# Optimization experiments

Measured on AMD Instinct MI355X. Metric: run time of the kernel, lower is better.

Reference implementation:

```python
import jax, jax.numpy as jnp
import numpy as np

D_MODEL = 512
NUM_HEADS = 8
NUM_REL_EMB = 1024


def _linear(x, w, b):
    # torch nn.Linear convention: w is [out, in]
    return x @ w.T + b


def setup_inputs() -> dict:
    key = jax.random.key(0)
    B, S, D = 1, 512, D_MODEL
    ks = jax.random.split(key, 14)
    scale = D ** -0.5
    def w(i):
        return jax.random.normal(ks[i], (D, D), jnp.float32) * scale
    def b(i):
        return jax.random.normal(ks[i], (D,), jnp.float32) * 0.01
    return {
        "hidden_states": jax.random.normal(ks[0], (B, S, D), jnp.float32),
        "emb_table": jax.random.normal(ks[1], (NUM_REL_EMB, D), jnp.float32) * 0.02,
        "wq": w(2), "bq": b(3),
        "wk": w(4), "bk": b(5),
        "wv": w(6), "bv": b(7),
        "wrk": w(8), "brk": b(9),
        "wrq": w(10), "brq": b(11),
        "wo": w(12), "bo": b(13),
    }


def reference(hidden_states, emb_table, wq, bq, wk, bk, wv, bv,
              wrk, brk, wrq, brq, wo, bo):
    B, S, D = hidden_states.shape
    H = NUM_HEADS
    hd = D // H
    NE = emb_table.shape[0]

    # relative positions j - i, shifted and clamped, then embedded: [S, S, D]
    rel_pos = jnp.arange(S)[None, :] - jnp.arange(S)[:, None]
    idx = jnp.clip(rel_pos + NE // 2, 0, NE - 1)
    rel_emb = emb_table[idx]  # [S, S, D] (identical across batch)

    q = _linear(hidden_states, wq, bq).reshape(B, S, H, hd).transpose(0, 2, 1, 3)  # [B,H,S,hd]
    k = _linear(hidden_states, wk, bk).reshape(B, S, H, hd).transpose(0, 2, 1, 3)
    v = _linear(hidden_states, wv, bv).reshape(B, S, H, hd).transpose(0, 2, 1, 3)

    rk = _linear(rel_emb, wrk, brk).reshape(S, S, H, hd)  # [i, j, H, hd]
    rq = _linear(rel_emb, wrq, brq).reshape(S, S, H, hd)

    # content-content + content-relative + relative-content scores: [B,H,S,S]
    scores = (
        jnp.einsum('bhid,bhjd->bhij', q, k)
        + jnp.einsum('bhid,ijhd->bhij', q, rk)
        + jnp.einsum('ijhd,bhjd->bhij', rq, k)
    )

    attn = jax.nn.softmax(scores / jnp.sqrt(jnp.asarray(hd, scores.dtype)), axis=-1)
    # dropout is identity (p=0.0 / eval mode)

    ctx = jnp.einsum('bhij,bhjd->bhid', attn, v)          # [B,H,S,hd]
    ctx = ctx.transpose(0, 2, 1, 3).reshape(B, S, D)       # merge heads
    out = _linear(ctx, wo, bo)
    return out, attn
```

## Files before the change

kernel.cpp:

```cpp
#include <hip/hip_runtime.h>
#include <stdint.h>


typedef __bf16 bf16_t;
typedef bf16_t bf16x8 __attribute__((ext_vector_type(8)));
typedef float f32x4 __attribute__((ext_vector_type(4)));
typedef float f32x2v __attribute__((ext_vector_type(2)));
typedef bf16_t bf16x2v __attribute__((ext_vector_type(2)));

__device__ __forceinline__ uint16_t f2bf(float f) {
  bf16_t b = (bf16_t)f;
  union { bf16_t b; uint16_t u; } c; c.b = b; return c.u;
}
__device__ __forceinline__ uint32_t cvt2(float lo, float hi) {
  bf16x2v v = __builtin_convertvector((f32x2v){lo, hi}, bf16x2v);
  union { bf16x2v v; uint32_t u; } c; c.v = v; return c.u;
}
__device__ __forceinline__ uint4 cvt8(float4 a, float4 b) {
  uint4 r;
  r.x = cvt2(a.x, a.y); r.y = cvt2(a.z, a.w);
  r.z = cvt2(b.x, b.y); r.w = cvt2(b.z, b.w);
  return r;
}
#define MFMA(a, b, c) __builtin_amdgcn_mfma_f32_16x16x32_bf16((a), (b), (c), 0, 0, 0)

#define LSTR 40
#define SSTR 72
#define RGN  13568

__global__ __launch_bounds__(256) void proj_kernel(
    const float* __restrict__ X, const float* __restrict__ emb,
    const float* __restrict__ wq, const float* __restrict__ bq,
    const float* __restrict__ wk, const float* __restrict__ bk,
    const float* __restrict__ wv, const float* __restrict__ bv,
    const float* __restrict__ wrk, const float* __restrict__ brk,
    const float* __restrict__ wrq, const float* __restrict__ brq,
    uint16_t* __restrict__ q, uint16_t* __restrict__ k, uint16_t* __restrict__ vT,
    uint16_t* __restrict__ rkE, uint16_t* __restrict__ rqE)
{
  int bid = blockIdx.x;
  const float *A, *B, *bias; uint16_t* C; int mode;
  if (bid < 64)       {            A = X;   B = wq;  bias = bq;  C = q;   mode = 2; }
  else if (bid < 128) { bid -= 64; A = X;   B = wk;  bias = bk;  C = k;   mode = 2; }
  else if (bid < 192) { bid -= 128; A = X;  B = wv;  bias = bv;  C = vT;  mode = 3; }
  else if (bid < 320) { bid -= 192; A = emb; B = wrk; bias = brk; C = rkE; mode = 1; }
  else                { bid -= 320; A = emb; B = wrq; bias = brq; C = rqE; mode = 1; }
  const int m0 = (bid >> 3) * 64, n0 = (bid & 7) * 64;

  __shared__ __align__(16) uint16_t As[64 * LSTR];
  __shared__ __align__(16) uint16_t Bs[64 * LSTR];
  const int t = threadIdx.x, lane = t & 63, wave = t >> 6;
  const int wi = wave & 1, wj = wave >> 1;
  const int quad = lane >> 4, l15 = lane & 15;
  const int srow = t >> 2, scol = (t & 3) * 8;

  const float* Af = A + (size_t)(m0 + srow) * 512 + scol;
  const float* Bf = B + (size_t)(n0 + srow) * 512 + scol;
  float4 a0 = *(const float4*)(Af), a1 = *(const float4*)(Af + 4);
  float4 b0 = *(const float4*)(Bf), b1 = *(const float4*)(Bf + 4);

  f32x4 acc[2][2] = {};
  for (int k0 = 0; k0 < 512; k0 += 32) {
    const uint4 ap = cvt8(a0, a1);
    const uint4 bp = cvt8(b0, b1);
    __syncthreads();
    *(uint4*)(&As[srow * LSTR + scol]) = ap;
    *(uint4*)(&Bs[srow * LSTR + scol]) = bp;
    __syncthreads();
    if (k0 < 480) {
      a0 = *(const float4*)(Af + k0 + 32); a1 = *(const float4*)(Af + k0 + 36);
      b0 = *(const float4*)(Bf + k0 + 32); b1 = *(const float4*)(Bf + k0 + 36);
    }
    bf16x8 af[2], bfr[2];
#pragma unroll
    for (int x = 0; x < 2; x++) {
      af[x]  = *(const bf16x8*)(&As[(wi * 32 + x * 16 + l15) * LSTR + quad * 8]);
      bfr[x] = *(const bf16x8*)(&Bs[(wj * 32 + x * 16 + l15) * LSTR + quad * 8]);
    }
#pragma unroll
    for (int x = 0; x < 2; x++)
#pragma unroll
      for (int y = 0; y < 2; y++)
        acc[x][y] = MFMA(af[x], bfr[y], acc[x][y]);
  }
#pragma unroll
  for (int x = 0; x < 2; x++)
#pragma unroll
    for (int y = 0; y < 2; y++) {
      const int j = n0 + wj * 32 + y * 16 + l15;
      const float bval = bias[j];
      const int ib = m0 + wi * 32 + x * 16 + quad * 4;
#pragma unroll
      for (int r = 0; r < 4; r++) {
        const int i = ib + r;
        size_t off;
        if (mode == 1)      off = (size_t)i * 512 + j;
        else if (mode == 2) off = (size_t)(j >> 6) * 32768 + (size_t)i * 64 + (size_t)(j & 63);
        else                off = (size_t)(j >> 6) * 32768 + (size_t)(j & 63) * 512 + (size_t)i;
        C[off] = f2bf(acc[x][y][r] + bval);
      }
    }
}

__global__ __launch_bounds__(512, 2) void attn_kernel(
    const uint16_t* __restrict__ q, const uint16_t* __restrict__ k,
    const uint16_t* __restrict__ rkE, const uint16_t* __restrict__ rqE,
    const uint16_t* __restrict__ vT,
    float* __restrict__ attn, uint16_t* __restrict__ ctx_bf)
{
  __shared__ __align__(16) char smem[8 * RGN + 1024];
  const int h = blockIdx.y, i0 = blockIdx.x * 16;
  const int t = threadIdx.x, lane = t & 63, w = t >> 6;
  const int quad = lane >> 4, l15 = lane & 15;
  const int j0 = w * 64;
  const int ebase = j0 - i0 + 497;

  char* rgn = smem + w * RGN;
  _Float16* U2h = (_Float16*)rgn;
  _Float16* U3h = (_Float16*)(rgn + 2688);
  uint16_t* Pw  = (uint16_t*)rgn;
  float*    ctxw = (float*)(rgn + 4096);
  float* rmax = (float*)(smem + 8 * RGN);
  float* rsum = rmax + 128;

  const uint16_t* qh = q  + (size_t)h * 32768;
  const uint16_t* kh = k  + (size_t)h * 32768;
  const uint16_t* vh = vT + (size_t)h * 32768;

  f32x4 acc1[4] = {}, acc2[5] = {}, acc3[5][4] = {};
#pragma unroll
  for (int s = 0; s < 2; s++) {
    const int ko = s * 32 + quad * 8;
    bf16x8 aq = *(const bf16x8*)(qh + (size_t)(i0 + l15) * 64 + ko);
    bf16x8 bk[4], arq[5], brk[5];
#pragma unroll
    for (int tt = 0; tt < 4; tt++)
      bk[tt] = *(const bf16x8*)(kh + (size_t)(j0 + tt * 16 + l15) * 64 + ko);
#pragma unroll
    for (int x = 0; x < 5; x++) {
      const int e = min(ebase + x * 16 + l15, 1023);
      arq[x] = *(const bf16x8*)(rqE + (size_t)e * 512 + h * 64 + ko);
      brk[x] = *(const bf16x8*)(rkE + (size_t)e * 512 + h * 64 + ko);
    }
#pragma unroll
    for (int tt = 0; tt < 4; tt++) acc1[tt] = MFMA(aq, bk[tt], acc1[tt]);
#pragma unroll
    for (int x = 0; x < 5; x++)    acc2[x] = MFMA(aq, brk[x], acc2[x]);
#pragma unroll
    for (int x = 0; x < 5; x++)
#pragma unroll
      for (int tt = 0; tt < 4; tt++) acc3[x][tt] = MFMA(arq[x], bk[tt], acc3[x][tt]);
  }
#pragma unroll
  for (int x = 0; x < 5; x++)
#pragma unroll
    for (int r = 0; r < 4; r++)
      U2h[(quad * 4 + r) * 84 + x * 16 + l15] = (_Float16)acc2[x][r];
#pragma unroll
  for (int x = 0; x < 5; x++)
#pragma unroll
    for (int tt = 0; tt < 4; tt++)
#pragma unroll
      for (int r = 0; r < 4; r++)
        U3h[(x * 16 + quad * 4 + r) * 68 + tt * 16 + l15] = (_Float16)acc3[x][tt][r];
  __syncthreads();

  f32x4 sc[4];
#pragma unroll
  for (int tt = 0; tt < 4; tt++)
#pragma unroll
    for (int r = 0; r < 4; r++) {
      const int ii = quad * 4 + r, jj = tt * 16 + l15;
      const int rb = jj - ii + 15;
      sc[tt][r] = (acc1[tt][r] + (float)U2h[ii * 84 + rb] + (float)U3h[rb * 68 + jj]) * 0.125f;
    }

  float mrow[4];
#pragma unroll
  for (int r = 0; r < 4; r++) {
    float m = fmaxf(fmaxf(sc[0][r], sc[1][r]), fmaxf(sc[2][r], sc[3][r]));
#pragma unroll
    for (int o = 1; o < 16; o <<= 1) m = fmaxf(m, __shfl_xor(m, o, 64));
    mrow[r] = m;
  }
  if (l15 == 0)
#pragma unroll
    for (int r = 0; r < 4; r++) rmax[w * 16 + quad * 4 + r] = mrow[r];
  __syncthreads();
  float srow[4];
#pragma unroll
  for (int r = 0; r < 4; r++) {
    const int row = quad * 4 + r;
    float m = rmax[row];
#pragma unroll
    for (int x = 1; x < 8; x++) m = fmaxf(m, rmax[x * 16 + row]);
    float s = 0.f;
#pragma unroll
    for (int tt = 0; tt < 4; tt++) {
      const float p = __expf(sc[tt][r] - m);
      sc[tt][r] = p; s += p;
    }
#pragma unroll
    for (int o = 1; o < 16; o <<= 1) s += __shfl_xor(s, o, 64);
    srow[r] = s;
  }
  if (l15 == 0)
#pragma unroll
    for (int r = 0; r < 4; r++) rsum[w * 16 + quad * 4 + r] = srow[r];
  __syncthreads();
#pragma unroll
  for (int r = 0; r < 4; r++) {
    const int row = quad * 4 + r;
    float s = rsum[row];
#pragma unroll
    for (int x = 1; x < 8; x++) s += rsum[x * 16 + row];
    const float inv = 1.0f / s;
#pragma unroll
    for (int tt = 0; tt < 4; tt++) {
      sc[tt][r] *= inv;
      attn[((size_t)h * 512 + i0 + row) * 512 + j0 + tt * 16 + l15] = sc[tt][r];
    }
  }

#pragma unroll
  for (int tt = 0; tt < 4; tt++)
#pragma unroll
    for (int r = 0; r < 4; r++)
      Pw[(quad * 4 + r) * SSTR + tt * 16 + l15] = f2bf(sc[tt][r]);
  __syncthreads();
  f32x4 apv[4] = {};
#pragma unroll
  for (int s = 0; s < 2; s++) {
    const int ko = s * 32 + quad * 8;
    bf16x8 aP = *(const bf16x8*)(&Pw[l15 * SSTR + ko]);
#pragma unroll
    for (int tt = 0; tt < 4; tt++) {
      bf16x8 bv = *(const bf16x8*)(vh + (size_t)(tt * 16 + l15) * 512 + j0 + ko);
      apv[tt] = MFMA(aP, bv, apv[tt]);
    }
  }
#pragma unroll
  for (int tt = 0; tt < 4; tt++)
#pragma unroll
    for (int r = 0; r < 4; r++)
      ctxw[(quad * 4 + r) * 64 + tt * 16 + l15] = apv[tt][r];
  __syncthreads();
  {
    const int idx = t * 2, row = idx >> 6, col = idx & 63;
    const size_t off = 4096 + (size_t)(row * 64 + col) * 4;
    float c0 = 0.f, c1 = 0.f;
#pragma unroll
    for (int x = 0; x < 8; x++) {
      float2 v = *(const float2*)(smem + x * RGN + off);
      c0 += v.x; c1 += v.y;
    }
    *(uint32_t*)(ctx_bf + (size_t)(i0 + row) * 512 + h * 64 + col) = cvt2(c0, c1);
  }
}

__global__ __launch_bounds__(256) void out_kernel(
    const uint16_t* __restrict__ ctx_bf, const float* __restrict__ wo,
    const float* __restrict__ bo, float* __restrict__ outp)
{
  __shared__ __align__(16) uint16_t As[32 * LSTR];
  __shared__ __align__(16) uint16_t Bs[64 * LSTR];
  const int m0 = blockIdx.y * 32, n0 = blockIdx.x * 64;
  const int t = threadIdx.x, lane = t & 63, wave = t >> 6;
  const int wm = wave & 1, wn = wave >> 1;
  const int quad = lane >> 4, l15 = lane & 15;
  const int srow = t >> 2, scol = (t & 3) * 8;

  const uint16_t* Af = ctx_bf + (size_t)(m0 + (srow & 31)) * 512 + scol;
  const float* Bf = wo + (size_t)(n0 + srow) * 512 + scol;
  uint4 ap = *(const uint4*)(Af);
  float4 b0 = *(const float4*)(Bf), b1 = *(const float4*)(Bf + 4);

  f32x4 acc[2] = {};
  for (int k0 = 0; k0 < 512; k0 += 32) {
    const uint4 bp = cvt8(b0, b1);
    const uint4 apc = ap;
    __syncthreads();
    if (t < 128) *(uint4*)(&As[srow * LSTR + scol]) = apc;
    *(uint4*)(&Bs[srow * LSTR + scol]) = bp;
    __syncthreads();
    if (k0 < 480) {
      ap = *(const uint4*)(Af + k0 + 32);
      b0 = *(const float4*)(Bf + k0 + 32); b1 = *(const float4*)(Bf + k0 + 36);
    }
    bf16x8 af = *(const bf16x8*)(&As[(wm * 16 + l15) * LSTR + quad * 8]);
#pragma unroll
    for (int y = 0; y < 2; y++) {
      bf16x8 bfr = *(const bf16x8*)(&Bs[(wn * 32 + y * 16 + l15) * LSTR + quad * 8]);
      acc[y] = MFMA(af, bfr, acc[y]);
    }
  }
#pragma unroll
  for (int y = 0; y < 2; y++) {
    const int j = n0 + wn * 32 + y * 16 + l15;
    const float bval = bo[j];
    const int ib = m0 + wm * 16 + quad * 4;
#pragma unroll
    for (int r = 0; r < 4; r++)
      outp[(size_t)(ib + r) * 512 + j] = acc[y][r] + bval;
  }
}

extern "C" void kernel_launch(void* const* d_in, const int* in_sizes, int n_in,
                              void* d_out, int out_size, void* d_ws, size_t ws_size,
                              hipStream_t stream) {
  const float* X   = (const float*)d_in[0];
  const float* emb = (const float*)d_in[1];
  const float* wq  = (const float*)d_in[2];
  const float* bq  = (const float*)d_in[3];
  const float* wk  = (const float*)d_in[4];
  const float* bk  = (const float*)d_in[5];
  const float* wv  = (const float*)d_in[6];
  const float* bv  = (const float*)d_in[7];
  const float* wrk = (const float*)d_in[8];
  const float* brk = (const float*)d_in[9];
  const float* wrq = (const float*)d_in[10];
  const float* brq = (const float*)d_in[11];
  const float* wo  = (const float*)d_in[12];
  const float* bo  = (const float*)d_in[13];

  uint16_t* q      = (uint16_t*)d_ws;
  uint16_t* k      = q   + 262144;
  uint16_t* vT     = k   + 262144;
  uint16_t* rkE    = vT  + 262144;
  uint16_t* rqE    = rkE + 524288;
  uint16_t* ctx_bf = rqE + 524288;

  float* outp = (float*)d_out;
  float* attn = (float*)d_out + 262144;

  proj_kernel<<<dim3(448), dim3(256), 0, stream>>>(X, emb, wq, bq, wk, bk, wv, bv,
                                                   wrk, brk, wrq, brq, q, k, vT, rkE, rqE);
  attn_kernel<<<dim3(32, 8), dim3(512), 0, stream>>>(q, k, rkE, rqE, vT, attn, ctx_bf);
  out_kernel<<<dim3(8, 16), dim3(256), 0, stream>>>(ctx_bf, wo, bo, outp);
}
```

Before: 120.1 us.

## Use single-wave register-direct GEMM tiles for projection and output kernels

The projection and output GEMMs drop the shared-memory staging and the block barriers. Each 64x64 tile is now computed by one wavefront that loads fp32 operands straight from global memory into MFMA fragments, with a 4x4 accumulator array per lane. This removes LDS traffic and __syncthreads, but cuts threads per tile from 256 to 64, drops the register prefetch, and launches the output GEMM with only 64 blocks. That risks lower latency hiding and poor occupancy on a large GPU.

Result: slower. 143.6 us (+19.6%).

```diff
diff --git a/kernel.cpp b/kernel.cpp
--- a/kernel.cpp
+++ b/kernel.cpp
@@ -16,19 +16,18 @@
   bf16x2v v = __builtin_convertvector((f32x2v){lo, hi}, bf16x2v);
   union { bf16x2v v; uint32_t u; } c; c.v = v; return c.u;
 }
-__device__ __forceinline__ uint4 cvt8(float4 a, float4 b) {
+__device__ __forceinline__ bf16x8 cvt8f(float4 a, float4 b) {
   uint4 r;
   r.x = cvt2(a.x, a.y); r.y = cvt2(a.z, a.w);
   r.z = cvt2(b.x, b.y); r.w = cvt2(b.z, b.w);
-  return r;
+  union { uint4 u; bf16x8 v; } c; c.u = r; return c.v;
 }
 #define MFMA(a, b, c) __builtin_amdgcn_mfma_f32_16x16x32_bf16((a), (b), (c), 0, 0, 0)
 
-#define LSTR 40
 #define SSTR 72
 #define RGN  13568
 
-__global__ __launch_bounds__(256) void proj_kernel(
+__global__ __launch_bounds__(64) void proj_kernel(
     const float* __restrict__ X, const float* __restrict__ emb,
     const float* __restrict__ wq, const float* __restrict__ bq,
     const float* __restrict__ wk, const float* __restrict__ bk,
@@ -38,58 +37,47 @@
     uint16_t* __restrict__ q, uint16_t* __restrict__ k, uint16_t* __restrict__ vT,
     uint16_t* __restrict__ rkE, uint16_t* __restrict__ rqE)
 {
-  int bid = blockIdx.x;
+  int v = blockIdx.x;
   const float *A, *B, *bias; uint16_t* C; int mode;
-  if (bid < 64)       {            A = X;   B = wq;  bias = bq;  C = q;   mode = 2; }
-  else if (bid < 128) { bid -= 64; A = X;   B = wk;  bias = bk;  C = k;   mode = 2; }
-  else if (bid < 192) { bid -= 128; A = X;  B = wv;  bias = bv;  C = vT;  mode = 3; }
-  else if (bid < 320) { bid -= 192; A = emb; B = wrk; bias = brk; C = rkE; mode = 1; }
-  else                { bid -= 320; A = emb; B = wrq; bias = brq; C = rqE; mode = 1; }
-  const int m0 = (bid >> 3) * 64, n0 = (bid & 7) * 64;
-
-  __shared__ __align__(16) uint16_t As[64 * LSTR];
-  __shared__ __align__(16) uint16_t Bs[64 * LSTR];
-  const int t = threadIdx.x, lane = t & 63, wave = t >> 6;
-  const int wi = wave & 1, wj = wave >> 1;
+  if (v < 64)       {           A = X;   B = wq;  bias = bq;  C = q;   mode = 2; }
+  else if (v < 128) { v -= 64;  A = X;   B = wk;  bias = bk;  C = k;   mode = 2; }
+  else if (v < 192) { v -= 128; A = X;   B = wv;  bias = bv;  C = vT;  mode = 3; }
+  else if (v < 320) { v -= 192; A = emb; B = wrk; bias = brk; C = rkE; mode = 1; }
+  else              { v -= 320; A = emb; B = wrq; bias = brq; C = rqE; mode = 1; }
+  const int m0 = (v >> 3) * 64, n0 = (v & 7) * 64;
+
+  const int lane = threadIdx.x & 63;
   const int quad = lane >> 4, l15 = lane & 15;
-  const int srow = t >> 2, scol = (t & 3) * 8;
-
-  const float* Af = A + (size_t)(m0 + srow) * 512 + scol;
-  const float* Bf = B + (size_t)(n0 + srow) * 512 + scol;
-  float4 a0 = *(const float4*)(Af), a1 = *(const float4*)(Af + 4);
-  float4 b0 = *(const float4*)(Bf), b1 = *(const float4*)(Bf + 4);
-
-  f32x4 acc[2][2] = {};
+
+  const float* Ab = A + (size_t)(m0 + l15) * 512 + quad * 8;
+  const float* Bb = B + (size_t)(n0 + l15) * 512 + quad * 8;
+
+  f32x4 acc[4][4] = {};
   for (int k0 = 0; k0 < 512; k0 += 32) {
-    const uint4 ap = cvt8(a0, a1);
-    const uint4 bp = cvt8(b0, b1);
-    __syncthreads();
-    *(uint4*)(&As[srow * LSTR + scol]) = ap;
-    *(uint4*)(&Bs[srow * LSTR + scol]) = bp;
-    __syncthreads();
-    if (k0 < 480) {
-      a0 = *(const float4*)(Af + k0 + 32); a1 = *(const float4*)(Af + k0 + 36);
-      b0 = *(const float4*)(Bf + k0 + 32); b1 = *(const float4*)(Bf + k0 + 36);
-    }
-    bf16x8 af[2], bfr[2];
-#pragma unroll
-    for (int x = 0; x < 2; x++) {
-      af[x]  = *(const bf16x8*)(&As[(wi * 32 + x * 16 + l15) * LSTR + quad * 8]);
-      bfr[x] = *(const bf16x8*)(&Bs[(wj * 32 + x * 16 + l15) * LSTR + quad * 8]);
-    }
-#pragma unroll
-    for (int x = 0; x < 2; x++)
-#pragma unroll
-      for (int y = 0; y < 2; y++)
+    bf16x8 af[4], bfr[4];
+#pragma unroll
+    for (int x = 0; x < 4; x++) {
+      const float* pa = Ab + (size_t)(x * 16) * 512 + k0;
+      af[x] = cvt8f(*(const float4*)pa, *(const float4*)(pa + 4));
+    }
+#pragma unroll
+    for (int y = 0; y < 4; y++) {
+      const float* pb = Bb + (size_t)(y * 16) * 512 + k0;
+      bfr[y] = cvt8f(*(const float4*)pb, *(const float4*)(pb + 4));
+    }
+#pragma unroll
+    for (int x = 0; x < 4; x++)
+#pragma unroll
+      for (int y = 0; y < 4; y++)
         acc[x][y] = MFMA(af[x], bfr[y], acc[x][y]);
   }
 #pragma unroll
-  for (int x = 0; x < 2; x++)
-#pragma unroll
-    for (int y = 0; y < 2; y++) {
-      const int j = n0 + wj * 32 + y * 16 + l15;
+  for (int x = 0; x < 4; x++)
+#pragma unroll
+    for (int y = 0; y < 4; y++) {
+      const int j = n0 + y * 16 + l15;
       const float bval = bias[j];
-      const int ib = m0 + wi * 32 + x * 16 + quad * 4;
+      const int ib = m0 + x * 16 + quad * 4;
 #pragma unroll
       for (int r = 0; r < 4; r++) {
         const int i = ib + r;
@@ -258,51 +246,45 @@
   }
 }
 
-__global__ __launch_bounds__(256) void out_kernel(
+__global__ __launch_bounds__(64) void out_kernel(
     const uint16_t* __restrict__ ctx_bf, const float* __restrict__ wo,
     const float* __restrict__ bo, float* __restrict__ outp)
 {
-  __shared__ __align__(16) uint16_t As[32 * LSTR];
-  __shared__ __align__(16) uint16_t Bs[64 * LSTR];
-  const int m0 = blockIdx.y * 32, n0 = blockIdx.x * 64;
-  const int t = threadIdx.x, lane = t & 63, wave = t >> 6;
-  const int wm = wave & 1, wn = wave >> 1;
+  const int m0 = (blockIdx.x >> 3) * 64, n0 = (blockIdx.x & 7) * 64;
+  const int lane = threadIdx.x & 63;
   const int quad = lane >> 4, l15 = lane & 15;
-  const int srow = t >> 2, scol = (t & 3) * 8;
-
-  const uint16_t* Af = ctx_bf + (size_t)(m0 + (srow & 31)) * 512 + scol;
-  const float* Bf = wo + (size_t)(n0 + srow) * 512 + scol;
-  uint4 ap = *(const uint4*)(Af);
-  float4 b0 = *(const float4*)(Bf), b1 = *(const float4*)(Bf + 4);
-
-  f32x4 acc[2] = {};
+
+  const uint16_t* Ab = ctx_bf + (size_t)(m0 + l15) * 512 + quad * 8;
+  const float* Bb = wo + (size_t)(n0 + l15) * 512 + quad * 8;
+
+  f32x4 acc[4][4] = {};
   for (int k0 = 0; k0 < 512; k0 += 32) {
-    const uint4 bp = cvt8(b0, b1);
-    const uint4 apc = ap;
-    __syncthreads();
-    if (t < 128) *(uint4*)(&As[srow * LSTR + scol]) = apc;
-    *(uint4*)(&Bs[srow * LSTR + scol]) = bp;
-    __syncthreads();
-    if (k0 < 480) {
-      ap = *(const uint4*)(Af + k0 + 32);
-      b0 = *(const float4*)(Bf + k0 + 32); b1 = *(const float4*)(Bf + k0 + 36);
-    }
-    bf16x8 af = *(const bf16x8*)(&As[(wm * 16 + l15) * LSTR + quad * 8]);
-#pragma unroll
-    for (int y = 0; y < 2; y++) {
-      bf16x8 bfr = *(const bf16x8*)(&Bs[(wn * 32 + y * 16 + l15) * LSTR + quad * 8]);
-      acc[y] = MFMA(af, bfr, acc[y]);
-    }
-  }
-#pragma unroll
-  for (int y = 0; y < 2; y++) {
-    const int j = n0 + wn * 32 + y * 16 + l15;
-    const float bval = bo[j];
-    const int ib = m0 + wm * 16 + quad * 4;
-#pragma unroll
-    for (int r = 0; r < 4; r++)
-      outp[(size_t)(ib + r) * 512 + j] = acc[y][r] + bval;
-  }
+    bf16x8 af[4], bfr[4];
+#pragma unroll
+    for (int x = 0; x < 4; x++)
+      af[x] = *(const bf16x8*)(Ab + (size_t)(x * 16) * 512 + k0);
+#pragma unroll
+    for (int y = 0; y < 4; y++) {
+      const float* pb = Bb + (size_t)(y * 16) * 512 + k0;
+      bfr[y] = cvt8f(*(const float4*)pb, *(const float4*)(pb + 4));
+    }
+#pragma unroll
+    for (int x = 0; x < 4; x++)
+#pragma unroll
+      for (int y = 0; y < 4; y++)
+        acc[x][y] = MFMA(af[x], bfr[y], acc[x][y]);
+  }
+#pragma unroll
+  for (int x = 0; x < 4; x++)
+#pragma unroll
+    for (int y = 0; y < 4; y++) {
+      const int j = n0 + y * 16 + l15;
+      const float bval = bo[j];
+      const int ib = m0 + x * 16 + quad * 4;
+#pragma unroll
+      for (int r = 0; r < 4; r++)
+        outp[(size_t)(ib + r) * 512 + j] = acc[x][y][r] + bval;
+    }
 }
 
 extern "C" void kernel_launch(void* const* d_in, const int* in_sizes, int n_in,
@@ -333,8 +315,8 @@
   float* outp = (float*)d_out;
   float* attn = (float*)d_out + 262144;
 
-  proj_kernel<<<dim3(448), dim3(256), 0, stream>>>(X, emb, wq, bq, wk, bk, wv, bv,
-                                                   wrk, brk, wrq, brq, q, k, vT, rkE, rqE);
+  proj_kernel<<<dim3(448), dim3(64), 0, stream>>>(X, emb, wq, bq, wk, bk, wv, bv,
+                                                  wrk, brk, wrq, brq, q, k, vT, rkE, rqE);
   attn_kernel<<<dim3(32, 8), dim3(512), 0, stream>>>(q, k, rkE, rqE, vT, attn, ctx_bf);
-  out_kernel<<<dim3(8, 16), dim3(256), 0, stream>>>(ctx_bf, wo, bo, outp);
-}
+  out_kernel<<<dim3(64), dim3(64), 0, stream>>>(ctx_bf, wo, bo, outp);
+}
```
